# Optimization experiments

Hardware: AMD Instinct MI355X
Metric: run time of the kernel (lower is better)

Reference implementation:

```python
import jax, jax.numpy as jnp
import numpy as np

E = 8      # n_routed_experts (== n_local)
K = 2      # n_activated_experts (top-k)
DIM = 2048
INTER = 1408
N_SHARED = 2
STD = 0.02


def setup_inputs() -> dict:
    key = jax.random.key(0)
    ks = jax.random.split(key, 9)
    B, S = 2, 2048
    return {
        "x": jax.random.normal(ks[0], (B, S, DIM), dtype=jnp.float32),
        "gate_w": jax.random.normal(ks[1], (E, DIM), dtype=jnp.float32) * STD,
        "router_bias": jnp.zeros((E,), dtype=jnp.float32),
        "W1": jax.random.normal(ks[2], (E, DIM, INTER), dtype=jnp.float32) * STD,
        "W3": jax.random.normal(ks[3], (E, DIM, INTER), dtype=jnp.float32) * STD,
        "W2": jax.random.normal(ks[4], (E, INTER, DIM), dtype=jnp.float32) * STD,
        "sw1": jax.random.normal(ks[5], (N_SHARED * INTER, DIM), dtype=jnp.float32) * STD,
        "sw3": jax.random.normal(ks[6], (N_SHARED * INTER, DIM), dtype=jnp.float32) * STD,
        "sw2": jax.random.normal(ks[7], (DIM, N_SHARED * INTER), dtype=jnp.float32) * STD,
    }


def reference(x, gate_w, router_bias, W1, W3, W2, sw1, sw3, sw2):
    B, S, D = x.shape
    X = x.reshape(-1, D)                       # [T, D]
    T = X.shape[0]

    # ---- Router: sigmoid scores, biased top-k selection, normalized weights
    logits = jnp.einsum('td,ed->te', X, gate_w)          # [T, E] (route_scale == 1.0)
    scores = jax.nn.sigmoid(logits)
    sel = scores + router_bias[None, :]
    _, idx = jax.lax.top_k(sel, K)                       # [T, K] int indices
    w = jnp.take_along_axis(scores, idx, axis=1)         # gather true scores
    w = w / jnp.clip(jnp.sum(w, axis=-1, keepdims=True), 1e-12)

    # Dense combine matrix [T, E]: gate weight where expert selected else 0
    gate_full = jnp.zeros((T, E), dtype=w.dtype).at[jnp.arange(T)[:, None], idx].set(w)

    # ---- Expert MLPs (SwiGLU) computed per-expert, combined by routing weight
    h1 = jnp.einsum('td,edh->eth', X, W1)                # [E, T, INTER]
    h3 = jnp.einsum('td,edh->eth', X, W3)
    y = jnp.einsum('eth,ehd->etd', jax.nn.silu(h1) * h3, W2)  # [E, T, D]
    out = jnp.einsum('etd,te->td', y, gate_full)         # weighted combine

    # ---- Shared expert MLP (always on)
    shared = jnp.einsum('th,dh->td',
                        jax.nn.silu(jnp.einsum('td,hd->th', X, sw1))
                        * jnp.einsum('td,hd->th', X, sw3), sw2)
    out = out + shared
    return out.reshape(B, S, D)
```

## Files before the change

### kernel.cpp

```cpp
#include <hip/hip_runtime.h>

#define DEV __device__ __forceinline__

typedef __attribute__((ext_vector_type(8))) short short8;
typedef __attribute__((ext_vector_type(4))) float floatx4;

constexpr int Tn  = 4096;
constexpr int Dm  = 2048;
constexpr int In  = 1408;
constexpr int En  = 8;
constexpr int SIn = 2816;
constexpr int CAP = 10240;

constexpr int SH_H = (Tn / 256) * (SIn / 128);
constexpr int SH_O = (Tn / 256) * (Dm / 256);
constexpr int NBLK = 256;

constexpr int RB  = Tn / 4;
constexpr int IB  = CAP / 256;
constexpr int CXB = Tn * Dm / 4 / 256;
constexpr int CWB = SIn * Dm / 4 / 256;
constexpr int TBZ = (Dm / 64) * (In / 64);
constexpr int O1 = RB;
constexpr int O2 = O1 + IB;
constexpr int O3 = O2 + CXB;
constexpr int O4 = O3 + CWB;
constexpr int O5 = O4 + CWB;
constexpr int O6 = O5 + CWB;
constexpr int PREP_B = O6 + TBZ * En * 3;

DEV unsigned short f2bf(float f) {
  unsigned int u = __float_as_uint(f);
  u += 0x7FFF + ((u >> 16) & 1);
  return (unsigned short)(u >> 16);
}

DEV float bf2f(unsigned short u) {
  return __uint_as_float(((unsigned int)u) << 16);
}

DEV void stg(const char* g, char* l) {
  __builtin_amdgcn_global_load_lds(
      (const __attribute__((address_space(1))) unsigned int*)g,
      (__attribute__((address_space(3))) unsigned int*)l, 16, 0, 0);
}

DEV unsigned ldsoff(const void* p) {
  return (unsigned)(unsigned long long)(__attribute__((address_space(3))) const char*)p;
}

#define BARR()  __builtin_amdgcn_s_barrier()
#define LGKM0() do { asm volatile("s_waitcnt lgkmcnt(0)" ::: "memory"); \
                     __builtin_amdgcn_sched_barrier(0); } while (0)
#define LGKM8() asm volatile("s_waitcnt lgkmcnt(8)" ::: "memory")
#define VMC(n)  asm volatile("s_waitcnt vmcnt(" #n ")" ::: "memory")
#define PRIO(x) __builtin_amdgcn_s_setprio(x)

#define DSR(dst, addr, OFFSTR) \
  asm volatile("ds_read_b128 %0, %1 offset:" OFFSTR : "=v"(dst) : "v"(addr))

#define RDA_LO(af, a) do { \
  DSR(af[0][0], a, "0");     DSR(af[0][1], a, "1024"); \
  DSR(af[1][0], a, "2048");  DSR(af[1][1], a, "3072"); \
  DSR(af[2][0], a, "4096");  DSR(af[2][1], a, "5120"); \
  DSR(af[3][0], a, "6144");  DSR(af[3][1], a, "7168"); } while (0)
#define RDA_HI(af, a) do { \
  DSR(af[0][0], a, "8192");  DSR(af[0][1], a, "9216"); \
  DSR(af[1][0], a, "10240"); DSR(af[1][1], a, "11264"); \
  DSR(af[2][0], a, "12288"); DSR(af[2][1], a, "13312"); \
  DSR(af[3][0], a, "14336"); DSR(af[3][1], a, "15360"); } while (0)
#define RDB_LO(bf, a) do { \
  DSR(bf[0][0], a, "0");    DSR(bf[0][1], a, "1024"); \
  DSR(bf[1][0], a, "2048"); DSR(bf[1][1], a, "3072"); } while (0)
#define RDB_HI(bf, a) do { \
  DSR(bf[2][0], a, "4096"); DSR(bf[2][1], a, "5120"); \
  DSR(bf[3][0], a, "6144"); DSR(bf[3][1], a, "7168"); } while (0)


__global__ void prep_kernel(const float* __restrict__ x,
                            const float* __restrict__ gw,
                            const float* __restrict__ bias,
                            const float* __restrict__ sw1,
                            const float* __restrict__ sw3,
                            const float* __restrict__ sw2,
                            const float* __restrict__ W1,
                            const float* __restrict__ W3,
                            const float* __restrict__ W2,
                            unsigned short* __restrict__ Xb,
                            unsigned short* __restrict__ sw1b,
                            unsigned short* __restrict__ sw3b,
                            unsigned short* __restrict__ sw2b,
                            unsigned short* __restrict__ W1t,
                            unsigned short* __restrict__ W3t,
                            unsigned short* __restrict__ W2t,
                            int* __restrict__ route_e,
                            float* __restrict__ route_w,
                            int* __restrict__ ptok) {
  __shared__ float tile[64][65];
  int bid = blockIdx.x;

  if (bid < O1) {
    int w = threadIdx.x >> 6, lane = threadIdx.x & 63;
    int t = bid * 4 + w;
    const float* xr = x + (long)t * Dm;
    double acc[En];
#pragma unroll
    for (int e = 0; e < En; e++) acc[e] = 0.0;
    for (int d = lane; d < Dm; d += 64) {
      double xv = (double)xr[d];
#pragma unroll
      for (int e = 0; e < En; e++) acc[e] += xv * (double)gw[e * Dm + d];
    }
#pragma unroll
    for (int off = 32; off > 0; off >>= 1) {
#pragma unroll
      for (int e = 0; e < En; e++) acc[e] += __shfl_down(acc[e], off);
    }
    if (lane == 0) {
      double sc[En], sel[En];
#pragma unroll
      for (int e = 0; e < En; e++) {
        sc[e] = 1.0 / (1.0 + exp(-acc[e]));
        sel[e] = sc[e] + (double)bias[e];
      }
      int i0 = 0;
#pragma unroll
      for (int e = 1; e < En; e++) if (sel[e] > sel[i0]) i0 = e;
      int i1 = (i0 == 0) ? 1 : 0;
#pragma unroll
      for (int e = 0; e < En; e++) if (e != i0 && sel[e] > sel[i1]) i1 = e;
      double s = sc[i0] + sc[i1];
      if (s < 1e-12) s = 1e-12;
      route_e[t * 2] = i0;  route_e[t * 2 + 1] = i1;
      route_w[t * 2] = (float)(sc[i0] / s);  route_w[t * 2 + 1] = (float)(sc[i1] / s);
    }
    return;
  }
  if (bid < O2) {
    int i = (bid - O1) * 256 + threadIdx.x;
    if (i < CAP) ptok[i] = 0;
    return;
  }
  if (bid < O6) {
    const float* src; unsigned short* dst; int i;
    if (bid < O3)      { src = x;   dst = Xb;   i = (bid - O2) * 256 + threadIdx.x; }
    else if (bid < O4) { src = sw1; dst = sw1b; i = (bid - O3) * 256 + threadIdx.x; }
    else if (bid < O5) { src = sw3; dst = sw3b; i = (bid - O4) * 256 + threadIdx.x; }
    else               { src = sw2; dst = sw2b; i = (bid - O5) * 256 + threadIdx.x; }
    float4 v = ((const float4*)src)[i];
    union { unsigned short u[4]; unsigned long long ll; } p;
    p.u[0] = f2bf(v.x); p.u[1] = f2bf(v.y); p.u[2] = f2bf(v.z); p.u[3] = f2bf(v.w);
    *(unsigned long long*)(dst + (long)i * 4) = p.ll;
    return;
  }
  int tb = bid - O6;
  int z = tb / (TBZ * En);
  int rem = tb % (TBZ * En);
  int y = rem / TBZ;
  int xb = rem % TBZ;
  const float* s0; unsigned short* d0; int R, C;
  if (z == 0)      { s0 = W1; d0 = W1t; R = Dm; C = In; }
  else if (z == 1) { s0 = W3; d0 = W3t; R = Dm; C = In; }
  else             { s0 = W2; d0 = W2t; R = In; C = Dm; }
  int tilesC = C >> 6;
  int tr = (xb / tilesC) << 6;
  int tc = (xb % tilesC) << 6;
  const float* s = s0 + (long)y * R * C;
  unsigned short* d = d0 + (long)y * R * C;
  int rr = threadIdx.x >> 4, c4 = (threadIdx.x & 15) << 2;
#pragma unroll
  for (int p = 0; p < 4; p++) {
    float4 v = *(const float4*)&s[(long)(tr + rr + 16 * p) * C + tc + c4];
    tile[rr + 16 * p][c4]     = v.x;
    tile[rr + 16 * p][c4 + 1] = v.y;
    tile[rr + 16 * p][c4 + 2] = v.z;
    tile[rr + 16 * p][c4 + 3] = v.w;
  }
  __syncthreads();
  int oc = threadIdx.x >> 5, i2 = (threadIdx.x & 31) << 1;
#pragma unroll
  for (int p = 0; p < 8; p++) {
    int j = oc + 8 * p;
    union { unsigned short u[2]; unsigned int w; } pk;
    pk.u[0] = f2bf(tile[i2][j]);
    pk.u[1] = f2bf(tile[i2 + 1][j]);
    *(unsigned int*)&d[(long)(tc + j) * R + tr + i2] = pk.w;
  }
}


__global__ void offscatter_kernel(const int* __restrict__ re,
                                  int* __restrict__ offs,
                                  int* __restrict__ ptok,
                                  int* __restrict__ pslot) {
  __shared__ int lcnt[En], loffs[En], lfill[En];
  int tid = threadIdx.x;
  if (tid < En) lcnt[tid] = 0;
  __syncthreads();
  for (int i = tid; i < Tn * 2; i += 1024) atomicAdd(&lcnt[re[i]], 1);
  __syncthreads();
  if (tid == 0) {
    int off = 0;
    for (int e = 0; e < En; e++) {
      loffs[e] = off; lfill[e] = off; offs[e] = off;
      off += (lcnt[e] + 255) & ~255;
    }
    offs[En] = off;
  }
  __syncthreads();
  for (int i = tid; i < Tn * 2; i += 1024) {
    int slot = atomicAdd(&lfill[re[i]], 1);
    ptok[slot] = i >> 1;
    pslot[i] = slot;
  }
}


DEV void mm16(floatx4 (&acc)[8][4], const short8 (&af)[4][2],
              const short8 (&bf)[4][2], int mq, int nq) {
#pragma unroll
  for (int i = 0; i < 4; i++)
#pragma unroll
    for (int n = 0; n < 2; n++)
#pragma unroll
      for (int kk = 0; kk < 2; kk++)
        acc[4 * mq + i][2 * nq + n] = __builtin_amdgcn_mfma_f32_16x16x32_bf16(
            af[i][kk], bf[2 * nq + n][kk], acc[4 * mq + i][2 * nq + n], 0, 0, 0);
}

DEV void chunk_rc(int c, int& rowh, int& colb) {
  rowh = ((c >> 7) << 4) | ((c >> 2) & 15);
  colb = (((c >> 6) & 1) << 6) | ((((c & 3) << 4)) ^ ((c & 32) ? 32 : 0));
}

DEV void gemm_core(char* LDS, const char* (&gA)[2][2], const char* (&gB)[2][2],
                   floatx4 (&acc)[8][4], int NT, int wm, int wn, int wv, int aswz) {
  const int bsel = (wn >> 1) * 16384 + ((wn & 1) << 13);
  const int wb = wv * 1024;
  unsigned base = ldsoff(LDS);
  unsigned aA0 = base + wm * 16384 + aswz;
  unsigned aB0 = base + 32768 + bsel + aswz;
  unsigned aA1 = aA0 + 65536, aB1 = aB0 + 65536;
  stg(gB[0][0], LDS + 32768 + wb);
  stg(gB[1][0], LDS + 32768 + 16384 + wb);
  stg(gB[0][1], LDS + 32768 + 8192 + wb);
  stg(gB[1][1], LDS + 32768 + 16384 + 8192 + wb);
  stg(gA[0][0], LDS + wb);
  stg(gA[1][0], LDS + 16384 + wb);
  stg(gA[0][1], LDS + 8192 + wb);
  stg(gA[1][1], LDS + 16384 + 8192 + wb);
  stg(gA[0][0] + 128, LDS + 65536 + wb);
  stg(gA[1][0] + 128, LDS + 65536 + 16384 + wb);
  stg(gB[0][0] + 128, LDS + 65536 + 32768 + wb);
  stg(gB[1][0] + 128, LDS + 65536 + 32768 + 16384 + wb);
  VMC(4);
  BARR();
  short8 af[4][2], bf[4][2];

  auto tile = [&](int t, int b, unsigned aA, unsigned aB) {
    char* An = LDS + ((b ^ 1) << 16);
    char* Bn = An + 32768;
    char* Ac = LDS + (b << 16);
    char* Bc = Ac + 32768;
    const int kn = (t + 1) << 7, ka = (t + 2) << 7;
    const bool s1 = (t + 1 < NT), s2 = (t + 2 < NT);
    RDA_LO(af, aA); RDB_LO(bf, aB);
    if (s1) { stg(gB[0][1] + kn, Bn + 8192 + wb);
              stg(gB[1][1] + kn, Bn + 16384 + 8192 + wb); }
    LGKM8(); BARR(); LGKM0(); PRIO(1); mm16(acc, af, bf, 0, 0); PRIO(0); BARR();
    RDB_HI(bf, aB);
    if (s1) { stg(gA[0][1] + kn, An + 8192 + wb);
              stg(gA[1][1] + kn, An + 16384 + 8192 + wb); }
    BARR(); LGKM0(); PRIO(1); mm16(acc, af, bf, 0, 1); PRIO(0); BARR();
    RDA_HI(af, aA);
    if (s2) { stg(gA[0][0] + ka, Ac + wb);
              stg(gA[1][0] + ka, Ac + 16384 + wb); }
    BARR(); LGKM0(); PRIO(1); mm16(acc, af, bf, 1, 0); PRIO(0); BARR();
    if (s2) { stg(gB[0][0] + ka, Bc + wb);
              stg(gB[1][0] + ka, Bc + 16384 + wb); }
    BARR(); LGKM0(); PRIO(1); mm16(acc, af, bf, 1, 1); PRIO(0);
    if (s2)      { VMC(4); }
    else if (s1) { VMC(0); }
    BARR();
  };
#pragma unroll 1
  for (int t2 = 0; t2 < NT; t2 += 2) {
    tile(t2, 0, aA0, aB0);
    tile(t2 + 1, 1, aA1, aB1);
  }
}


DEV void h_body(const unsigned short* Xb, const unsigned short* B1p,
                const unsigned short* B3p, unsigned short* ap, int Nact,
                int m0, int n0, const int* ptok, bool routed, char* LDS) {
  int tid = threadIdx.x, wv = tid >> 6, lane = tid & 63;
  int wm = wv >> 2, wn = wv & 3;
  int fr = lane & 15, fq = lane >> 4;
  int aswz = fr * 64 + ((fq * 16) ^ ((fr & 8) << 2));

  const char* gA[2][2]; const char* gB[2][2];
#pragma unroll
  for (int j = 0; j < 2; j++) {
    int rowh, colb;
    chunk_rc(j * 512 + tid, rowh, colb);
#pragma unroll
    for (int h = 0; h < 2; h++) {
      int grA = m0 + h * 128 + rowh;
      long ra = routed ? (long)ptok[grA] : (long)grA;
      gA[h][j] = (const char*)Xb + ra * (long)(Dm * 2) + colb;
      int rt = h * 128 + rowh;
      const unsigned short* src = ((rt >> 5) & 1) ? B3p : B1p;
      long rb = (long)n0 + ((rt >> 6) << 5) + (rt & 31);
      gB[h][j] = (const char*)src + rb * (long)(Dm * 2) + colb;
    }
  }
  floatx4 acc[8][4];
#pragma unroll
  for (int i = 0; i < 8; i++)
#pragma unroll
    for (int n = 0; n < 4; n++) acc[i][n] = (floatx4)0.0f;

  gemm_core(LDS, gA, gB, acc, Dm / 64, wm, wn, wv, aswz);

#pragma unroll
  for (int mi = 0; mi < 8; mi++)
#pragma unroll
    for (int n = 0; n < 2; n++)
#pragma unroll
      for (int r = 0; r < 4; r++) {
        int row = m0 + wm * 128 + mi * 16 + fq * 4 + r;
        int col = n0 + wn * 32 + n * 16 + fr;
        float h1 = acc[mi][n][r], h3 = acc[mi][n + 2][r];
        float v = h1 / (1.0f + __expf(-h1)) * h3;
        ap[(long)row * Nact + col] = f2bf(v);
      }
}

__global__ __launch_bounds__(512, 1)
void h_all(const unsigned short* __restrict__ Xb,
           const unsigned short* __restrict__ W1t,
           const unsigned short* __restrict__ W3t,
           const unsigned short* __restrict__ sw1b,
           const unsigned short* __restrict__ sw3b,
           unsigned short* __restrict__ act,
           unsigned short* __restrict__ actS,
           const int* __restrict__ ptok,
           const int* __restrict__ offs) {
  extern __shared__ char LDS[];
  const int Mr = offs[En] >> 8;
  const int RT = Mr * (In / 128);
  const int TT = RT + SH_H;
  const int per = (TT + 7) >> 3;
  const int xcd = blockIdx.x & 7, lix = blockIdx.x >> 3;
#pragma unroll 1
  for (int i = lix; i < per; i += 32) {
    int t = xcd * per + i;
    if (t >= TT) break;
    if (t < RT) {
      int m0 = (t % Mr) * 256, n0 = (t / Mr) * 128;
      int e = 0;
      while (!(m0 >= offs[e] && m0 < offs[e + 1])) e++;
      h_body(Xb, W1t + (long)e * In * Dm, W3t + (long)e * In * Dm,
             act, In, m0, n0, ptok, true, LDS);
    } else {
      int u = t - RT;
      int m0 = (u & 15) * 256, n0 = (u >> 4) * 128;
      h_body(Xb, sw1b, sw3b, actS, SIn, m0, n0, nullptr, false, LDS);
    }
  }
}


DEV void o_core(const unsigned short* Apt, const unsigned short* Bpt,
                int lda, int ldb, int NT, int m0, int n0,
                floatx4 (&acc)[8][4], char* LDS) {
  int tid = threadIdx.x, wv = tid >> 6, lane = tid & 63;
  int wm = wv >> 2, wn = wv & 3;
  int fr = lane & 15, fq = lane >> 4;
  int aswz = fr * 64 + ((fq * 16) ^ ((fr & 8) << 2));

  const char* gA[2][2]; const char* gB[2][2];
#pragma unroll
  for (int j = 0; j < 2; j++) {
    int rowh, colb;
    chunk_rc(j * 512 + tid, rowh, colb);
#pragma unroll
    for (int h = 0; h < 2; h++) {
      gA[h][j] = (const char*)Apt + (long)(m0 + h * 128 + rowh) * (lda * 2) + colb;
      gB[h][j] = (const char*)Bpt + (long)(n0 + h * 128 + rowh) * (ldb * 2) + colb;
    }
  }
#pragma unroll
  for (int i = 0; i < 8; i++)
#pragma unroll
    for (int n = 0; n < 4; n++) acc[i][n] = (floatx4)0.0f;

  gemm_core(LDS, gA, gB, acc, NT, wm, wn, wv, aswz);
}

__global__ __launch_bounds__(512, 1)
void o_all(const unsigned short* __restrict__ act,
           const unsigned short* __restrict__ actS,
           const unsigned short* __restrict__ W2t,
           const unsigned short* __restrict__ sw2b,
           unsigned short* __restrict__ yR,
           float* __restrict__ out,
           const int* __restrict__ offs) {
  extern __shared__ char LDS[];
  const int Mr = offs[En] >> 8;
  const int RT = Mr * (Dm / 256);
  const int TT = SH_O + RT;
  int lane = threadIdx.x & 63, wv = threadIdx.x >> 6;
  int wm = wv >> 2, wn = wv & 3;
  int fr = lane & 15, fq = lane >> 4;
  const int per = (TT + 7) >> 3;
  const int xcd = blockIdx.x & 7, lix = blockIdx.x >> 3;
#pragma unroll 1
  for (int i = lix; i < per; i += 32) {
    int t = xcd * per + i;
    if (t >= TT) break;
    floatx4 acc[8][4];
    if (t >= SH_O) {
      int u = t - SH_O;
      int m0 = (u % Mr) * 256, n0 = (u / Mr) * 256;
      int e = 0;
      while (!(m0 >= offs[e] && m0 < offs[e + 1])) e++;
      o_core(act, W2t + (long)e * Dm * In, In, In, In / 64, m0, n0, acc, LDS);
#pragma unroll
      for (int mi = 0; mi < 8; mi++)
#pragma unroll
        for (int r = 0; r < 4; r++) {
          int row = m0 + wm * 128 + mi * 16 + fq * 4 + r;
#pragma unroll
          for (int ni = 0; ni < 4; ni++) {
            int col = n0 + wn * 64 + ni * 16 + fr;
            yR[(long)row * Dm + col] = f2bf(acc[mi][ni][r]);
          }
        }
    } else {
      int u = t;
      int m0 = (u & 15) * 256, n0 = (u >> 4) * 256;
      o_core(actS, sw2b, SIn, SIn, SIn / 64, m0, n0, acc, LDS);
#pragma unroll
      for (int mi = 0; mi < 8; mi++)
#pragma unroll
        for (int r = 0; r < 4; r++) {
          int row = m0 + wm * 128 + mi * 16 + fq * 4 + r;
#pragma unroll
          for (int ni = 0; ni < 4; ni++) {
            int col = n0 + wn * 64 + ni * 16 + fr;
            out[(long)row * Dm + col] = acc[mi][ni][r];
          }
        }
    }
  }
}


__global__ void combine_kernel(const unsigned short* __restrict__ yR,
                               const int* __restrict__ pslot,
                               const float* __restrict__ rw,
                               float* __restrict__ out) {
  int idx = blockIdx.x * 256 + threadIdx.x;
  int t = idx >> 9, c4 = idx & 511;
  int s0 = pslot[t * 2], s1 = pslot[t * 2 + 1];
  float w0 = rw[t * 2], w1 = rw[t * 2 + 1];
  ushort4 a = ((const ushort4*)(yR + (long)s0 * Dm))[c4];
  ushort4 b = ((const ushort4*)(yR + (long)s1 * Dm))[c4];
  float4* op = (float4*)(out + (long)t * Dm) + c4;
  float4 o = *op;
  o.x += w0 * bf2f(a.x) + w1 * bf2f(b.x);
  o.y += w0 * bf2f(a.y) + w1 * bf2f(b.y);
  o.z += w0 * bf2f(a.z) + w1 * bf2f(b.z);
  o.w += w0 * bf2f(a.w) + w1 * bf2f(b.w);
  *op = o;
}


extern "C" void kernel_launch(void* const* d_in, const int* in_sizes, int n_in,
                              void* d_out, int out_size, void* d_ws, size_t ws_size,
                              hipStream_t stream) {
  const float* x    = (const float*)d_in[0];
  const float* gw   = (const float*)d_in[1];
  const float* bias = (const float*)d_in[2];
  const float* W1   = (const float*)d_in[3];
  const float* W3   = (const float*)d_in[4];
  const float* W2   = (const float*)d_in[5];
  const float* sw1  = (const float*)d_in[6];
  const float* sw3  = (const float*)d_in[7];
  const float* sw2  = (const float*)d_in[8];
  float* out = (float*)d_out;

  static bool attr_done = false;
  if (!attr_done) {
    hipFuncSetAttribute(reinterpret_cast<const void*>(h_all),
                        hipFuncAttributeMaxDynamicSharedMemorySize, 131072);
    hipFuncSetAttribute(reinterpret_cast<const void*>(o_all),
                        hipFuncAttributeMaxDynamicSharedMemorySize, 131072);
    attr_done = true;
  }

  char* p = (char*)d_ws;
  auto alloc = [&](size_t bytes) {
    char* r = p; p += (bytes + 255) & ~(size_t)255; return r;
  };
  unsigned short* Xb   = (unsigned short*)alloc((size_t)Tn * Dm * 2);
  unsigned short* W1t  = (unsigned short*)alloc((size_t)En * In * Dm * 2);
  unsigned short* W3t  = (unsigned short*)alloc((size_t)En * In * Dm * 2);
  unsigned short* W2t  = (unsigned short*)alloc((size_t)En * Dm * In * 2);
  unsigned short* sw1b = (unsigned short*)alloc((size_t)SIn * Dm * 2);
  unsigned short* sw3b = (unsigned short*)alloc((size_t)SIn * Dm * 2);
  unsigned short* sw2b = (unsigned short*)alloc((size_t)Dm * SIn * 2);
  unsigned short* act  = (unsigned short*)alloc((size_t)CAP * In * 2);
  unsigned short* actS = (unsigned short*)alloc((size_t)Tn * SIn * 2);
  unsigned short* yR   = (unsigned short*)alloc((size_t)CAP * Dm * 2);
  int*   route_e = (int*)alloc(Tn * 2 * 4);
  float* route_w = (float*)alloc(Tn * 2 * 4);
  int*   offs    = (int*)alloc(256);
  int*   ptok    = (int*)alloc(CAP * 4);
  int*   pslot   = (int*)alloc(Tn * 2 * 4);

  prep_kernel<<<PREP_B, 256, 0, stream>>>(
      x, gw, bias, sw1, sw3, sw2, W1, W3, W2,
      Xb, sw1b, sw3b, sw2b, W1t, W3t, W2t, route_e, route_w, ptok);

  offscatter_kernel<<<1, 1024, 0, stream>>>(route_e, offs, ptok, pslot);

  h_all<<<NBLK, 512, 131072, stream>>>(Xb, W1t, W3t, sw1b, sw3b, act, actS, ptok, offs);
  o_all<<<NBLK, 512, 131072, stream>>>(act, actS, W2t, sw2b, yR, out, offs);

  combine_kernel<<<Tn * (Dm / 4) / 256, 256, 0, stream>>>(yR, pslot, route_w, out);
}
```

Measured before the change: 703.9 us.

## Fuse all MoE stages into one cooperative persistent kernel with grid syncs

Replaces the five separate launches (prep, offset scatter, h GEMM, o GEMM, combine) with a single cooperative kernel of 256 blocks that uses grid.sync between phases. The prep and combine phases become grid-stride loops, and the router runs with 8 warps per block. The aim is to remove launch gaps and tail idling between kernels. In exchange, the prep phase now runs at one 512-thread block per CU with no overlap between blocks, and the offset scatter runs on a single block while the rest of the grid waits. A fallback to separate kernels is kept in case the cooperative launch fails.

```diff
diff --git a/kernel.cpp b/kernel.cpp
--- a/kernel.cpp
+++ b/kernel.cpp
@@ -1,4 +1,7 @@
 #include <hip/hip_runtime.h>
+#include <hip/hip_cooperative_groups.h>
+
+namespace cg = cooperative_groups;
 
 #define DEV __device__ __forceinline__
 
@@ -15,19 +18,8 @@
 constexpr int SH_H = (Tn / 256) * (SIn / 128);
 constexpr int SH_O = (Tn / 256) * (Dm / 256);
 constexpr int NBLK = 256;
-
-constexpr int RB  = Tn / 4;
-constexpr int IB  = CAP / 256;
-constexpr int CXB = Tn * Dm / 4 / 256;
-constexpr int CWB = SIn * Dm / 4 / 256;
-constexpr int TBZ = (Dm / 64) * (In / 64);
-constexpr int O1 = RB;
-constexpr int O2 = O1 + IB;
-constexpr int O3 = O2 + CXB;
-constexpr int O4 = O3 + CWB;
-constexpr int O5 = O4 + CWB;
-constexpr int O6 = O5 + CWB;
-constexpr int PREP_B = O6 + TBZ * En * 3;
+constexpr int GSTR = NBLK * 512;
+constexpr int TTILES = (Dm / 64) * (In / 64) * En * 3;
 
 DEV unsigned short f2bf(float f) {
   unsigned int u = __float_as_uint(f);
@@ -77,141 +69,44 @@
   DSR(bf[3][0], a, "6144"); DSR(bf[3][1], a, "7168"); } while (0)
 
 
-__global__ void prep_kernel(const float* __restrict__ x,
-                            const float* __restrict__ gw,
-                            const float* __restrict__ bias,
-                            const float* __restrict__ sw1,
-                            const float* __restrict__ sw3,
-                            const float* __restrict__ sw2,
-                            const float* __restrict__ W1,
-                            const float* __restrict__ W3,
-                            const float* __restrict__ W2,
-                            unsigned short* __restrict__ Xb,
-                            unsigned short* __restrict__ sw1b,
-                            unsigned short* __restrict__ sw3b,
-                            unsigned short* __restrict__ sw2b,
-                            unsigned short* __restrict__ W1t,
-                            unsigned short* __restrict__ W3t,
-                            unsigned short* __restrict__ W2t,
-                            int* __restrict__ route_e,
-                            float* __restrict__ route_w,
-                            int* __restrict__ ptok) {
-  __shared__ float tile[64][65];
-  int bid = blockIdx.x;
-
-  if (bid < O1) {
-    int w = threadIdx.x >> 6, lane = threadIdx.x & 63;
-    int t = bid * 4 + w;
-    const float* xr = x + (long)t * Dm;
-    double acc[En];
-#pragma unroll
-    for (int e = 0; e < En; e++) acc[e] = 0.0;
-    for (int d = lane; d < Dm; d += 64) {
-      double xv = (double)xr[d];
-#pragma unroll
-      for (int e = 0; e < En; e++) acc[e] += xv * (double)gw[e * Dm + d];
-    }
-#pragma unroll
-    for (int off = 32; off > 0; off >>= 1) {
-#pragma unroll
-      for (int e = 0; e < En; e++) acc[e] += __shfl_down(acc[e], off);
-    }
-    if (lane == 0) {
-      double sc[En], sel[En];
-#pragma unroll
-      for (int e = 0; e < En; e++) {
-        sc[e] = 1.0 / (1.0 + exp(-acc[e]));
-        sel[e] = sc[e] + (double)bias[e];
-      }
-      int i0 = 0;
-#pragma unroll
-      for (int e = 1; e < En; e++) if (sel[e] > sel[i0]) i0 = e;
-      int i1 = (i0 == 0) ? 1 : 0;
-#pragma unroll
-      for (int e = 0; e < En; e++) if (e != i0 && sel[e] > sel[i1]) i1 = e;
-      double s = sc[i0] + sc[i1];
-      if (s < 1e-12) s = 1e-12;
-      route_e[t * 2] = i0;  route_e[t * 2 + 1] = i1;
-      route_w[t * 2] = (float)(sc[i0] / s);  route_w[t * 2 + 1] = (float)(sc[i1] / s);
-    }
-    return;
-  }
-  if (bid < O2) {
-    int i = (bid - O1) * 256 + threadIdx.x;
-    if (i < CAP) ptok[i] = 0;
-    return;
-  }
-  if (bid < O6) {
-    const float* src; unsigned short* dst; int i;
-    if (bid < O3)      { src = x;   dst = Xb;   i = (bid - O2) * 256 + threadIdx.x; }
-    else if (bid < O4) { src = sw1; dst = sw1b; i = (bid - O3) * 256 + threadIdx.x; }
-    else if (bid < O5) { src = sw3; dst = sw3b; i = (bid - O4) * 256 + threadIdx.x; }
-    else               { src = sw2; dst = sw2b; i = (bid - O5) * 256 + threadIdx.x; }
+DEV void cvt4(const float* __restrict__ src, unsigned short* __restrict__ dst,
+              int n4, int gtid) {
+#pragma unroll 1
+  for (int i = gtid; i < n4; i += GSTR) {
     float4 v = ((const float4*)src)[i];
     union { unsigned short u[4]; unsigned long long ll; } p;
     p.u[0] = f2bf(v.x); p.u[1] = f2bf(v.y); p.u[2] = f2bf(v.z); p.u[3] = f2bf(v.w);
     *(unsigned long long*)(dst + (long)i * 4) = p.ll;
-    return;
-  }
-  int tb = bid - O6;
-  int z = tb / (TBZ * En);
-  int rem = tb % (TBZ * En);
-  int y = rem / TBZ;
-  int xb = rem % TBZ;
-  const float* s0; unsigned short* d0; int R, C;
-  if (z == 0)      { s0 = W1; d0 = W1t; R = Dm; C = In; }
-  else if (z == 1) { s0 = W3; d0 = W3t; R = Dm; C = In; }
-  else             { s0 = W2; d0 = W2t; R = In; C = Dm; }
+  }
+}
+
+DEV void transpose_tile(const float* __restrict__ s0, unsigned short* __restrict__ d0,
+                        int R, int C, int y, int xb, char* LDSC) {
+  float (*tile)[65] = (float(*)[65])LDSC;
   int tilesC = C >> 6;
-  int tr = (xb / tilesC) << 6;
-  int tc = (xb % tilesC) << 6;
+  int tr = (xb / tilesC) << 6, tc = (xb % tilesC) << 6;
   const float* s = s0 + (long)y * R * C;
   unsigned short* d = d0 + (long)y * R * C;
-  int rr = threadIdx.x >> 4, c4 = (threadIdx.x & 15) << 2;
+  int tid = threadIdx.x;
+  int rr = tid >> 4, c4 = (tid & 15) << 2;
+  __syncthreads();
+#pragma unroll
+  for (int p = 0; p < 2; p++) {
+    float4 v = *(const float4*)&s[(long)(tr + rr + 32 * p) * C + tc + c4];
+    tile[rr + 32 * p][c4]     = v.x;
+    tile[rr + 32 * p][c4 + 1] = v.y;
+    tile[rr + 32 * p][c4 + 2] = v.z;
+    tile[rr + 32 * p][c4 + 3] = v.w;
+  }
+  __syncthreads();
+  int oc = tid >> 5, i2 = (tid & 31) << 1;
 #pragma unroll
   for (int p = 0; p < 4; p++) {
-    float4 v = *(const float4*)&s[(long)(tr + rr + 16 * p) * C + tc + c4];
-    tile[rr + 16 * p][c4]     = v.x;
-    tile[rr + 16 * p][c4 + 1] = v.y;
-    tile[rr + 16 * p][c4 + 2] = v.z;
-    tile[rr + 16 * p][c4 + 3] = v.w;
-  }
-  __syncthreads();
-  int oc = threadIdx.x >> 5, i2 = (threadIdx.x & 31) << 1;
-#pragma unroll
-  for (int p = 0; p < 8; p++) {
-    int j = oc + 8 * p;
+    int j = oc + 16 * p;
     union { unsigned short u[2]; unsigned int w; } pk;
     pk.u[0] = f2bf(tile[i2][j]);
     pk.u[1] = f2bf(tile[i2 + 1][j]);
     *(unsigned int*)&d[(long)(tc + j) * R + tr + i2] = pk.w;
-  }
-}
-
-
-__global__ void offscatter_kernel(const int* __restrict__ re,
-                                  int* __restrict__ offs,
-                                  int* __restrict__ ptok,
-                                  int* __restrict__ pslot) {
-  __shared__ int lcnt[En], loffs[En], lfill[En];
-  int tid = threadIdx.x;
-  if (tid < En) lcnt[tid] = 0;
-  __syncthreads();
-  for (int i = tid; i < Tn * 2; i += 1024) atomicAdd(&lcnt[re[i]], 1);
-  __syncthreads();
-  if (tid == 0) {
-    int off = 0;
-    for (int e = 0; e < En; e++) {
-      loffs[e] = off; lfill[e] = off; offs[e] = off;
-      off += (lcnt[e] + 255) & ~255;
-    }
-    offs[En] = off;
-  }
-  __syncthreads();
-  for (int i = tid; i < Tn * 2; i += 1024) {
-    int slot = atomicAdd(&lfill[re[i]], 1);
-    ptok[slot] = i >> 1;
-    pslot[i] = slot;
   }
 }
 
@@ -337,17 +232,11 @@
       }
 }
 
-__global__ __launch_bounds__(512, 1)
-void h_all(const unsigned short* __restrict__ Xb,
-           const unsigned short* __restrict__ W1t,
-           const unsigned short* __restrict__ W3t,
-           const unsigned short* __restrict__ sw1b,
-           const unsigned short* __restrict__ sw3b,
-           unsigned short* __restrict__ act,
-           unsigned short* __restrict__ actS,
-           const int* __restrict__ ptok,
-           const int* __restrict__ offs) {
-  extern __shared__ char LDS[];
+DEV void h_phase(const unsigned short* Xb, const unsigned short* W1t,
+                 const unsigned short* W3t, const unsigned short* sw1b,
+                 const unsigned short* sw3b, unsigned short* act,
+                 unsigned short* actS, const int* ptok, const int* offs,
+                 char* LDS) {
   const int Mr = offs[En] >> 8;
   const int RT = Mr * (In / 128);
   const int TT = RT + SH_H;
@@ -399,15 +288,9 @@
   gemm_core(LDS, gA, gB, acc, NT, wm, wn, wv, aswz);
 }
 
-__global__ __launch_bounds__(512, 1)
-void o_all(const unsigned short* __restrict__ act,
-           const unsigned short* __restrict__ actS,
-           const unsigned short* __restrict__ W2t,
-           const unsigned short* __restrict__ sw2b,
-           unsigned short* __restrict__ yR,
-           float* __restrict__ out,
-           const int* __restrict__ offs) {
-  extern __shared__ char LDS[];
+DEV void o_phase(const unsigned short* act, const unsigned short* actS,
+                 const unsigned short* W2t, const unsigned short* sw2b,
+                 unsigned short* yR, float* out, const int* offs, char* LDS) {
   const int Mr = offs[En] >> 8;
   const int RT = Mr * (Dm / 256);
   const int TT = SH_O + RT;
@@ -458,10 +341,221 @@
 }
 
 
-__global__ void combine_kernel(const unsigned short* __restrict__ yR,
-                               const int* __restrict__ pslot,
-                               const float* __restrict__ rw,
-                               float* __restrict__ out) {
+DEV void router_body(const float* x, const float* gw, const float* bias,
+                     int* route_e, float* route_w) {
+  int wv = threadIdx.x >> 6, lane = threadIdx.x & 63;
+#pragma unroll 1
+  for (int t = blockIdx.x * 8 + wv; t < Tn; t += NBLK * 8) {
+    const float* xr = x + (long)t * Dm;
+    double acc[En];
+#pragma unroll
+    for (int e = 0; e < En; e++) acc[e] = 0.0;
+    for (int d = lane; d < Dm; d += 64) {
+      double xv = (double)xr[d];
+#pragma unroll
+      for (int e = 0; e < En; e++) acc[e] += xv * (double)gw[e * Dm + d];
+    }
+#pragma unroll
+    for (int off = 32; off > 0; off >>= 1) {
+#pragma unroll
+      for (int e = 0; e < En; e++) acc[e] += __shfl_down(acc[e], off);
+    }
+    if (lane == 0) {
+      double sc[En], sel[En];
+#pragma unroll
+      for (int e = 0; e < En; e++) {
+        sc[e] = 1.0 / (1.0 + exp(-acc[e]));
+        sel[e] = sc[e] + (double)bias[e];
+      }
+      int i0 = 0;
+#pragma unroll
+      for (int e = 1; e < En; e++) if (sel[e] > sel[i0]) i0 = e;
+      int i1 = (i0 == 0) ? 1 : 0;
+#pragma unroll
+      for (int e = 0; e < En; e++) if (e != i0 && sel[e] > sel[i1]) i1 = e;
+      double s = sc[i0] + sc[i1];
+      if (s < 1e-12) s = 1e-12;
+      route_e[t * 2] = i0;  route_e[t * 2 + 1] = i1;
+      route_w[t * 2] = (float)(sc[i0] / s);  route_w[t * 2 + 1] = (float)(sc[i1] / s);
+    }
+  }
+}
+
+
+__global__ __launch_bounds__(512, 1)
+void moe_mega(const float* __restrict__ x, const float* __restrict__ gw,
+              const float* __restrict__ bias,
+              const float* __restrict__ sw1, const float* __restrict__ sw3,
+              const float* __restrict__ sw2,
+              const float* __restrict__ W1, const float* __restrict__ W3,
+              const float* __restrict__ W2,
+              unsigned short* __restrict__ Xb,
+              unsigned short* __restrict__ sw1b, unsigned short* __restrict__ sw3b,
+              unsigned short* __restrict__ sw2b,
+              unsigned short* __restrict__ W1t, unsigned short* __restrict__ W3t,
+              unsigned short* __restrict__ W2t,
+              unsigned short* __restrict__ act, unsigned short* __restrict__ actS,
+              unsigned short* __restrict__ yR,
+              int* __restrict__ route_e, float* __restrict__ route_w,
+              int* __restrict__ offs, int* __restrict__ ptok,
+              int* __restrict__ pslot, float* __restrict__ out) {
+  extern __shared__ char LDS[];
+  cg::grid_group grid = cg::this_grid();
+  int gtid = blockIdx.x * 512 + threadIdx.x;
+
+  router_body(x, gw, bias, route_e, route_w);
+  if (gtid < CAP) ptok[gtid] = 0;
+  cvt4(x,   Xb,   Tn * Dm / 4, gtid);
+  cvt4(sw1, sw1b, SIn * Dm / 4, gtid);
+  cvt4(sw3, sw3b, SIn * Dm / 4, gtid);
+  cvt4(sw2, sw2b, Dm * SIn / 4, gtid);
+  {
+    const int TBZ = (Dm / 64) * (In / 64);
+#pragma unroll 1
+    for (int tb = blockIdx.x; tb < TTILES; tb += NBLK) {
+      int z = tb / (TBZ * En);
+      int rem = tb % (TBZ * En);
+      int y = rem / TBZ, xb = rem % TBZ;
+      if (z == 0)      transpose_tile(W1, W1t, Dm, In, y, xb, LDS);
+      else if (z == 1) transpose_tile(W3, W3t, Dm, In, y, xb, LDS);
+      else             transpose_tile(W2, W2t, In, Dm, y, xb, LDS);
+    }
+  }
+  __threadfence();
+  grid.sync();
+
+  if (blockIdx.x == 0) {
+    int* lcnt  = (int*)LDS;
+    int* lfill = lcnt + En;
+    int tid = threadIdx.x;
+    if (tid < En) lcnt[tid] = 0;
+    __syncthreads();
+    for (int i = tid; i < Tn * 2; i += 512) atomicAdd(&lcnt[route_e[i]], 1);
+    __syncthreads();
+    if (tid == 0) {
+      int off = 0;
+      for (int e = 0; e < En; e++) {
+        offs[e] = off; lfill[e] = off;
+        off += (lcnt[e] + 255) & ~255;
+      }
+      offs[En] = off;
+    }
+    __syncthreads();
+    for (int i = tid; i < Tn * 2; i += 512) {
+      int slot = atomicAdd(&lfill[route_e[i]], 1);
+      ptok[slot] = i >> 1;
+      pslot[i] = slot;
+    }
+  }
+  __threadfence();
+  grid.sync();
+
+  h_phase(Xb, W1t, W3t, sw1b, sw3b, act, actS, ptok, offs, LDS);
+  __threadfence();
+  grid.sync();
+
+  o_phase(act, actS, W2t, sw2b, yR, out, offs, LDS);
+  __threadfence();
+  grid.sync();
+
+#pragma unroll 1
+  for (int idx = gtid; idx < Tn * (Dm / 4); idx += GSTR) {
+    int t = idx >> 9, c4 = idx & 511;
+    int s0 = pslot[t * 2], s1 = pslot[t * 2 + 1];
+    float w0 = route_w[t * 2], w1 = route_w[t * 2 + 1];
+    ushort4 a = ((const ushort4*)(yR + (long)s0 * Dm))[c4];
+    ushort4 b = ((const ushort4*)(yR + (long)s1 * Dm))[c4];
+    float4* op = (float4*)(out + (long)t * Dm) + c4;
+    float4 o = *op;
+    o.x += w0 * bf2f(a.x) + w1 * bf2f(b.x);
+    o.y += w0 * bf2f(a.y) + w1 * bf2f(b.y);
+    o.z += w0 * bf2f(a.z) + w1 * bf2f(b.z);
+    o.w += w0 * bf2f(a.w) + w1 * bf2f(b.w);
+    *op = o;
+  }
+}
+
+
+__global__ void fb_prep(const float* __restrict__ x, const float* __restrict__ gw,
+                        const float* __restrict__ bias,
+                        const float* __restrict__ sw1, const float* __restrict__ sw3,
+                        const float* __restrict__ sw2,
+                        const float* __restrict__ W1, const float* __restrict__ W3,
+                        const float* __restrict__ W2,
+                        unsigned short* __restrict__ Xb,
+                        unsigned short* __restrict__ sw1b, unsigned short* __restrict__ sw3b,
+                        unsigned short* __restrict__ sw2b,
+                        unsigned short* __restrict__ W1t, unsigned short* __restrict__ W3t,
+                        unsigned short* __restrict__ W2t,
+                        int* __restrict__ route_e, float* __restrict__ route_w,
+                        int* __restrict__ ptok) {
+  __shared__ char SL[64 * 65 * 4];
+  int gtid = blockIdx.x * 512 + threadIdx.x;
+  router_body(x, gw, bias, route_e, route_w);
+  if (gtid < CAP) ptok[gtid] = 0;
+  cvt4(x,   Xb,   Tn * Dm / 4, gtid);
+  cvt4(sw1, sw1b, SIn * Dm / 4, gtid);
+  cvt4(sw3, sw3b, SIn * Dm / 4, gtid);
+  cvt4(sw2, sw2b, Dm * SIn / 4, gtid);
+  const int TBZ = (Dm / 64) * (In / 64);
+#pragma unroll 1
+  for (int tb = blockIdx.x; tb < TTILES; tb += NBLK) {
+    int z = tb / (TBZ * En);
+    int rem = tb % (TBZ * En);
+    int y = rem / TBZ, xb = rem % TBZ;
+    if (z == 0)      transpose_tile(W1, W1t, Dm, In, y, xb, SL);
+    else if (z == 1) transpose_tile(W3, W3t, Dm, In, y, xb, SL);
+    else             transpose_tile(W2, W2t, In, Dm, y, xb, SL);
+  }
+}
+
+__global__ void fb_offscatter(const int* __restrict__ re, int* __restrict__ offs,
+                              int* __restrict__ ptok, int* __restrict__ pslot) {
+  __shared__ int lcnt[En], lfill[En];
+  int tid = threadIdx.x;
+  if (tid < En) lcnt[tid] = 0;
+  __syncthreads();
+  for (int i = tid; i < Tn * 2; i += 1024) atomicAdd(&lcnt[re[i]], 1);
+  __syncthreads();
+  if (tid == 0) {
+    int off = 0;
+    for (int e = 0; e < En; e++) {
+      offs[e] = off; lfill[e] = off;
+      off += (lcnt[e] + 255) & ~255;
+    }
+    offs[En] = off;
+  }
+  __syncthreads();
+  for (int i = tid; i < Tn * 2; i += 1024) {
+    int slot = atomicAdd(&lfill[re[i]], 1);
+    ptok[slot] = i >> 1;
+    pslot[i] = slot;
+  }
+}
+
+__global__ __launch_bounds__(512, 1)
+void fb_h(const unsigned short* __restrict__ Xb, const unsigned short* __restrict__ W1t,
+          const unsigned short* __restrict__ W3t, const unsigned short* __restrict__ sw1b,
+          const unsigned short* __restrict__ sw3b, unsigned short* __restrict__ act,
+          unsigned short* __restrict__ actS, const int* __restrict__ ptok,
+          const int* __restrict__ offs) {
+  extern __shared__ char LDS[];
+  h_phase(Xb, W1t, W3t, sw1b, sw3b, act, actS, ptok, offs, LDS);
+}
+
+__global__ __launch_bounds__(512, 1)
+void fb_o(const unsigned short* __restrict__ act, const unsigned short* __restrict__ actS,
+          const unsigned short* __restrict__ W2t, const unsigned short* __restrict__ sw2b,
+          unsigned short* __restrict__ yR, float* __restrict__ out,
+          const int* __restrict__ offs) {
+  extern __shared__ char LDS[];
+  o_phase(act, actS, W2t, sw2b, yR, out, offs, LDS);
+}
+
+__global__ void fb_combine(const unsigned short* __restrict__ yR,
+                           const int* __restrict__ pslot,
+                           const float* __restrict__ rw,
+                           float* __restrict__ out) {
   int idx = blockIdx.x * 256 + threadIdx.x;
   int t = idx >> 9, c4 = idx & 511;
   int s0 = pslot[t * 2], s1 = pslot[t * 2 + 1];
@@ -494,9 +588,11 @@
 
   static bool attr_done = false;
   if (!attr_done) {
-    hipFuncSetAttribute(reinterpret_cast<const void*>(h_all),
+    hipFuncSetAttribute(reinterpret_cast<const void*>(moe_mega),
                         hipFuncAttributeMaxDynamicSharedMemorySize, 131072);
-    hipFuncSetAttribute(reinterpret_cast<const void*>(o_all),
+    hipFuncSetAttribute(reinterpret_cast<const void*>(fb_h),
+                        hipFuncAttributeMaxDynamicSharedMemorySize, 131072);
+    hipFuncSetAttribute(reinterpret_cast<const void*>(fb_o),
                         hipFuncAttributeMaxDynamicSharedMemorySize, 131072);
     attr_done = true;
   }
@@ -521,14 +617,26 @@
   int*   ptok    = (int*)alloc(CAP * 4);
   int*   pslot   = (int*)alloc(Tn * 2 * 4);
 
-  prep_kernel<<<PREP_B, 256, 0, stream>>>(
-      x, gw, bias, sw1, sw3, sw2, W1, W3, W2,
-      Xb, sw1b, sw3b, sw2b, W1t, W3t, W2t, route_e, route_w, ptok);
-
-  offscatter_kernel<<<1, 1024, 0, stream>>>(route_e, offs, ptok, pslot);
-
-  h_all<<<NBLK, 512, 131072, stream>>>(Xb, W1t, W3t, sw1b, sw3b, act, actS, ptok, offs);
-  o_all<<<NBLK, 512, 131072, stream>>>(act, actS, W2t, sw2b, yR, out, offs);
-
-  combine_kernel<<<Tn * (Dm / 4) / 256, 256, 0, stream>>>(yR, pslot, route_w, out);
-}
+  void* args[] = {
+    (void*)&x, (void*)&gw, (void*)&bias, (void*)&sw1, (void*)&sw3, (void*)&sw2,
+    (void*)&W1, (void*)&W3, (void*)&W2,
+    (void*)&Xb, (void*)&sw1b, (void*)&sw3b, (void*)&sw2b,
+    (void*)&W1t, (void*)&W3t, (void*)&W2t,
+    (void*)&act, (void*)&actS, (void*)&yR,
+    (void*)&route_e, (void*)&route_w, (void*)&offs, (void*)&ptok, (void*)&pslot,
+    (void*)&out
+  };
+  hipError_t err = hipLaunchCooperativeKernel(
+      reinterpret_cast<const void*>(moe_mega), dim3(NBLK), dim3(512),
+      args, 131072, stream);
+
+  if (err != hipSuccess) {
+    fb_prep<<<NBLK, 512, 0, stream>>>(x, gw, bias, sw1, sw3, sw2, W1, W3, W2,
+                                      Xb, sw1b, sw3b, sw2b, W1t, W3t, W2t,
+                                      route_e, route_w, ptok);
+    fb_offscatter<<<1, 1024, 0, stream>>>(route_e, offs, ptok, pslot);
+    fb_h<<<NBLK, 512, 131072, stream>>>(Xb, W1t, W3t, sw1b, sw3b, act, actS, ptok, offs);
+    fb_o<<<NBLK, 512, 131072, stream>>>(act, actS, W2t, sw2b, yR, out, offs);
+    fb_combine<<<Tn * (Dm / 4) / 256, 256, 0, stream>>>(yR, pslot, route_w, out);
+  }
+}
```

Result: slower. 1.150 ms (+63.4%).
